# Performance work log

Measured on AMD Instinct MI355X. Metric: run time of the kernel, lower is better.

Reference implementation:

```python
import jax, jax.numpy as jnp
import numpy as np

N_HEAD = 16

def setup_inputs() -> dict:
    key = jax.random.key(0)
    k1, k2, k3 = jax.random.split(key, 3)
    B, T, C = 2, 2048, 2048
    x = jax.random.normal(k1, (B, T, C), dtype=jnp.float32)
    # torch Linear weights are [out, in]; init with small scale for stability
    w_attn = jax.random.normal(k2, (3 * C, C), dtype=jnp.float32) * 0.02
    b_attn = jnp.zeros((3 * C,), dtype=jnp.float32)
    w_proj = jax.random.normal(k3, (C, C), dtype=jnp.float32) * 0.02
    b_proj = jnp.zeros((C,), dtype=jnp.float32)
    return {"x": x, "w_attn": w_attn, "b_attn": b_attn, "w_proj": w_proj, "b_proj": b_proj}

def reference(x, w_attn, b_attn, w_proj, b_proj):
    B, T, C = x.shape
    nh = N_HEAD
    hs = C // nh
    # fused QKV projection (torch Linear: x @ W^T + b)
    qkv = x @ w_attn.T + b_attn                      # [B, T, 3C]
    q, k, v = jnp.split(qkv, 3, axis=2)
    # [B, nh, T, hs]
    q = q.reshape(B, T, nh, hs).transpose(0, 2, 1, 3)
    k = k.reshape(B, T, nh, hs).transpose(0, 2, 1, 3)
    v = v.reshape(B, T, nh, hs).transpose(0, 2, 1, 3)
    # causal scaled dot-product attention
    scale = 1.0 / jnp.sqrt(jnp.asarray(hs, dtype=x.dtype))
    logits = jnp.einsum("bhqd,bhkd->bhqk", q, k) * scale  # [B, nh, T, T]
    causal = jnp.tril(jnp.ones((T, T), dtype=bool))
    logits = jnp.where(causal, logits, jnp.finfo(logits.dtype).min)
    attn = jax.nn.softmax(logits, axis=-1)
    y = jnp.einsum("bhqk,bhkd->bhqd", attn, v)       # [B, nh, T, hs]
    y = y.transpose(0, 2, 1, 3).reshape(B, T, C)
    # output projection (resid_dropout is identity in eval / p=0)
    y = y @ w_proj.T + b_proj
    return y
```

## Files before the change

### kernel.cpp

```cpp
#include <hip/hip_runtime.h>
#include <stdint.h>

typedef __bf16 bf16_t;
typedef __bf16 bf16x8 __attribute__((ext_vector_type(8)));
typedef float f32x4 __attribute__((ext_vector_type(4)));
typedef unsigned short us16x8 __attribute__((ext_vector_type(8)));

#define MFMA16(a, b, c) __builtin_amdgcn_mfma_f32_16x16x32_bf16(a, b, c, 0, 0, 0)

__device__ __forceinline__ void stage16(const bf16_t* g, bf16_t* l) {
#if __has_builtin(__builtin_amdgcn_global_load_lds)
  __builtin_amdgcn_global_load_lds((__attribute__((address_space(1))) void*)g,
                                   (__attribute__((address_space(3))) void*)l, 16, 0, 0);
#else
  *(bf16x8*)l = *(const bf16x8*)g;
#endif
}

__global__ __launch_bounds__(256) void cvt_f32_to_bf16(const float* __restrict__ in,
                                                       bf16_t* __restrict__ out, int n8) {
  int i = blockIdx.x * 256 + threadIdx.x;
  if (i >= n8) return;
  const f32x4* p = (const f32x4*)(in + (size_t)i * 8);
  f32x4 a = p[0], b = p[1];
  bf16x8 o;
  o[0] = (bf16_t)a[0]; o[1] = (bf16_t)a[1]; o[2] = (bf16_t)a[2]; o[3] = (bf16_t)a[3];
  o[4] = (bf16_t)b[0]; o[5] = (bf16_t)b[1]; o[6] = (bf16_t)b[2]; o[7] = (bf16_t)b[3];
  *(bf16x8*)(out + (size_t)i * 8) = o;
}

template <int OUT_BF16>
__global__ __launch_bounds__(256) void gemm_nt(const bf16_t* __restrict__ A,
                                               const bf16_t* __restrict__ B,
                                               const float* __restrict__ bias,
                                               void* __restrict__ Cout,
                                               int M, int N, int K) {
  __shared__ bf16_t As[128 * 64];
  __shared__ bf16_t Bs[128 * 64];
  int tid = threadIdx.x;
  int l = tid & 63, w = tid >> 6;
  int wr = w >> 1, wc = w & 1;
  int nbn = N >> 7;
  int bm = blockIdx.x / nbn, bn = blockIdx.x % nbn;
  int l15 = l & 15, l4 = l >> 4, l7 = l & 7;

  f32x4 acc[4][4] = {};

  for (int ks = 0; ks < K; ks += 64) {
#pragma unroll
    for (int i = 0; i < 4; ++i) {
      int e = i * 256 + tid;
      int row = e >> 3, blk = e & 7;
      int col = ks + ((blk ^ (row & 7)) << 3);
      stage16(A + (size_t)(bm * 128 + row) * K + col, As + e * 8);
      stage16(B + (size_t)(bn * 128 + row) * K + col, Bs + e * 8);
    }
    __syncthreads();
#pragma unroll
    for (int kk = 0; kk < 2; ++kk) {
      bf16x8 af[4], bfr[4];
      int blk = (kk * 4 + l4) ^ l7;
#pragma unroll
      for (int m = 0; m < 4; ++m) {
        af[m] = *(const bf16x8*)(As + (wr * 64 + m * 16 + l15) * 64 + blk * 8);
        bfr[m] = *(const bf16x8*)(Bs + (wc * 64 + m * 16 + l15) * 64 + blk * 8);
      }
#pragma unroll
      for (int m = 0; m < 4; ++m)
#pragma unroll
        for (int n = 0; n < 4; ++n)
          acc[m][n] = MFMA16(af[m], bfr[n], acc[m][n]);
    }
    __syncthreads();
  }

  int rbase = bm * 128 + wr * 64 + (l4 << 2);
  int cbase = bn * 128 + wc * 64 + l15;
#pragma unroll
  for (int n = 0; n < 4; ++n) {
    float bv = bias[cbase + n * 16];
#pragma unroll
    for (int m = 0; m < 4; ++m)
#pragma unroll
      for (int r = 0; r < 4; ++r) {
        float v = acc[m][n][r] + bv;
        size_t off = (size_t)(rbase + m * 16 + r) * N + (cbase + n * 16);
        if (OUT_BF16) ((bf16_t*)Cout)[off] = (bf16_t)v;
        else ((float*)Cout)[off] = v;
      }
  }
}

__global__ __launch_bounds__(256, 2) void attn_fwd(const bf16_t* __restrict__ qkv,
                                                   bf16_t* __restrict__ att) {
  __shared__ bf16_t Kt[64 * 128];
  __shared__ bf16_t Vt[128 * 64];
  __shared__ bf16_t Pw[4][16 * 64];

  int bid = blockIdx.x;
  int pair = bid >> 5, bh = bid & 31;
  int h = bh & 15, b = bh >> 4;
  int tid = threadIdx.x;
  int l = tid & 63, w = tid >> 6;
  int l15 = l & 15, l4 = l >> 4, l7 = l & 7;
  const size_t LD = 6144;
  const bf16_t* base = qkv + (size_t)b * 2048 * LD;

#pragma unroll 1
  for (int phase = 0; phase < 2; ++phase) {
    int qt = phase ? 31 - pair : pair;
    int q0 = qt << 6;
    int wq0 = q0 + w * 16;

    bf16x8 qf[4];
#pragma unroll
    for (int kk = 0; kk < 4; ++kk)
      qf[kk] = *(const bf16x8*)(base + (size_t)(wq0 + l15) * LD + h * 128 + kk * 32 + l4 * 8);

    f32x4 acc[8] = {};
    float mrow[4], lrow[4];
#pragma unroll
    for (int r = 0; r < 4; ++r) { mrow[r] = -1e30f; lrow[r] = 0.f; }

    int nkt = qt + 1;
    for (int kt = 0; kt < nkt; ++kt) {
      int kb = kt << 6;
      const bf16_t* vg = base + (size_t)kb * LD + 4096 + h * 128;
      us16x8 va[2], vb[2];
#pragma unroll
      for (int p = 0; p < 2; ++p) {
        int g = p * 256 + tid;
        int kv = (g >> 4) << 1;
        int d0 = (g & 15) << 3;
        va[p] = *(const us16x8*)(vg + (size_t)kv * LD + d0);
        vb[p] = *(const us16x8*)(vg + (size_t)(kv + 1) * LD + d0);
      }
      const bf16_t* kg = base + (size_t)kb * LD + 2048 + h * 128;
#pragma unroll
      for (int i = 0; i < 4; ++i) {
        int e = i * 256 + tid;
        int row = e >> 4, blk = e & 15;
        int src = (blk ^ (row & 7)) << 3;
        stage16(kg + (size_t)row * LD + src, Kt + e * 8);
      }
#pragma unroll
      for (int p = 0; p < 2; ++p) {
        int g = p * 256 + tid;
        int kv = (g >> 4) << 1;
        int d0 = (g & 15) << 3;
        int k8 = kv >> 3, kr = kv & 7;
#pragma unroll
        for (int j = 0; j < 8; ++j) {
          int d = d0 + j;
          int swz = k8 ^ ((d ^ (d >> 3)) & 7);
          unsigned pack = (unsigned)va[p][j] | ((unsigned)vb[p][j] << 16);
          *(unsigned*)(&Vt[d * 64 + swz * 8 + kr]) = pack;
        }
      }
      __syncthreads();

      f32x4 s[4] = {};
      __builtin_amdgcn_s_setprio(1);
#pragma unroll
      for (int kk = 0; kk < 4; ++kk) {
        int blk = (kk * 4 + l4) ^ l7;
#pragma unroll
        for (int n = 0; n < 4; ++n) {
          bf16x8 kf = *(const bf16x8*)(Kt + (n * 16 + l15) * 128 + blk * 8);
          s[n] = MFMA16(qf[kk], kf, s[n]);
        }
      }
      __builtin_amdgcn_s_setprio(0);

      const float sc = 0.08838834764831845f;
      bool needMask = (kb + 63) > wq0;
      float scf[4];
#pragma unroll
      for (int r = 0; r < 4; ++r) {
        int q = wq0 + (l4 << 2) + r;
#pragma unroll
        for (int n = 0; n < 4; ++n) {
          float v = s[n][r] * sc;
          if (needMask && (kb + n * 16 + l15) > q) v = -1e30f;
          s[n][r] = v;
        }
        float mx = fmaxf(fmaxf(s[0][r], s[1][r]), fmaxf(s[2][r], s[3][r]));
        mx = fmaxf(mx, __shfl_xor(mx, 1));
        mx = fmaxf(mx, __shfl_xor(mx, 2));
        mx = fmaxf(mx, __shfl_xor(mx, 4));
        mx = fmaxf(mx, __shfl_xor(mx, 8));
        float mn = fmaxf(mrow[r], mx);
        float sf = __expf(mrow[r] - mn);
        mrow[r] = mn;
        scf[r] = sf;
        float rs = 0.f;
#pragma unroll
        for (int n = 0; n < 4; ++n) {
          float pv = __expf(s[n][r] - mn);
          s[n][r] = pv;
          rs += pv;
        }
        rs += __shfl_xor(rs, 1);
        rs += __shfl_xor(rs, 2);
        rs += __shfl_xor(rs, 4);
        rs += __shfl_xor(rs, 8);
        lrow[r] = lrow[r] * sf + rs;
      }
#pragma unroll
      for (int nd = 0; nd < 8; ++nd)
#pragma unroll
        for (int r = 0; r < 4; ++r)
          acc[nd][r] *= scf[r];
#pragma unroll
      for (int n = 0; n < 4; ++n) {
        int cb8 = n * 2 + (l15 >> 3);
#pragma unroll
        for (int r = 0; r < 4; ++r) {
          int row = (l4 << 2) + r;
          Pw[w][row * 64 + ((cb8 ^ (row & 7)) << 3) + l7] = (bf16_t)s[n][r];
        }
      }
      __builtin_amdgcn_s_setprio(1);
#pragma unroll
      for (int kk2 = 0; kk2 < 2; ++kk2) {
        bf16x8 pa = *(const bf16x8*)(&Pw[w][l15 * 64 + (((kk2 * 4 + l4) ^ l7) << 3)]);
#pragma unroll
        for (int nd = 0; nd < 8; ++nd) {
          int d = nd * 16 + l15;
          int swz = (kk2 * 4 + l4) ^ ((d ^ (d >> 3)) & 7);
          bf16x8 bv = *(const bf16x8*)(&Vt[d * 64 + swz * 8]);
          acc[nd] = MFMA16(pa, bv, acc[nd]);
        }
      }
      __builtin_amdgcn_s_setprio(0);
      __syncthreads();
    }

#pragma unroll
    for (int r = 0; r < 4; ++r) {
      float inv = 1.0f / lrow[r];
      size_t ro = (size_t)(b * 2048 + wq0 + (l4 << 2) + r) * 2048 + h * 128;
#pragma unroll
      for (int nd = 0; nd < 8; ++nd)
        att[ro + nd * 16 + l15] = (bf16_t)(acc[nd][r] * inv);
    }
  }
}

extern "C" void kernel_launch(void* const* d_in, const int* in_sizes, int n_in,
                              void* d_out, int out_size, void* d_ws, size_t ws_size,
                              hipStream_t stream) {
  (void)in_sizes; (void)n_in; (void)out_size; (void)ws_size;
  const float* x = (const float*)d_in[0];
  const float* w_attn = (const float*)d_in[1];
  const float* b_attn = (const float*)d_in[2];
  const float* w_proj = (const float*)d_in[3];
  const float* b_proj = (const float*)d_in[4];
  float* out = (float*)d_out;

  char* ws = (char*)d_ws;
  bf16_t* xb  = (bf16_t*)(ws);
  bf16_t* wab = (bf16_t*)(ws + 16777216);
  bf16_t* wpb = (bf16_t*)(ws + 41943040);
  bf16_t* qkv = (bf16_t*)(ws + 50331648);
  bf16_t* att = xb;

  cvt_f32_to_bf16<<<4096, 256, 0, stream>>>(x, xb, 1048576);
  cvt_f32_to_bf16<<<6144, 256, 0, stream>>>(w_attn, wab, 1572864);
  cvt_f32_to_bf16<<<2048, 256, 0, stream>>>(w_proj, wpb, 524288);

  gemm_nt<1><<<32 * 48, 256, 0, stream>>>(xb, wab, b_attn, qkv, 4096, 6144, 2048);

  attn_fwd<<<512, 256, 0, stream>>>(qkv, att);

  gemm_nt<0><<<32 * 16, 256, 0, stream>>>(att, wpb, b_proj, out, 4096, 2048, 2048);
}
```

Before: 287.0 us.

## Add 256x256 eight-wave ping-pong GEMM for QKV projection

Replaces the 128x128-tile QKV GEMM with a new 512-thread kernel using 256x256 tiles, double-buffered LDS staged through global_load_lds, and explicit barrier, waitcnt and priority scheduling. Each K step is split into quarter phases so async loads of the next tiles overlap MFMA work. Workgroup IDs are also remapped across eight groups for better cache locality. The aim is higher MFMA utilisation and fewer global loads per FLOP. In exchange it uses about 128 KB of LDS per block, relies on hand-tuned vmcnt values being correct, and the attention block change is only scoping.

```diff
diff --git a/kernel.cpp b/kernel.cpp
--- a/kernel.cpp
+++ b/kernel.cpp
@@ -7,14 +7,23 @@
 typedef unsigned short us16x8 __attribute__((ext_vector_type(8)));
 
 #define MFMA16(a, b, c) __builtin_amdgcn_mfma_f32_16x16x32_bf16(a, b, c, 0, 0, 0)
+#define BAR() __builtin_amdgcn_s_barrier()
+#define PRIO1() __builtin_amdgcn_s_setprio(1)
+#define PRIO0() __builtin_amdgcn_s_setprio(0)
+#define LGKM0()                                       \
+  do {                                                \
+    asm volatile("s_waitcnt lgkmcnt(0)" ::: "memory"); \
+    __builtin_amdgcn_sched_barrier(0);                \
+  } while (0)
+#define VMCNT(n)                                             \
+  do {                                                       \
+    asm volatile("s_waitcnt vmcnt(" #n ")" ::: "memory");    \
+    __builtin_amdgcn_sched_barrier(0);                       \
+  } while (0)
 
 __device__ __forceinline__ void stage16(const bf16_t* g, bf16_t* l) {
-#if __has_builtin(__builtin_amdgcn_global_load_lds)
   __builtin_amdgcn_global_load_lds((__attribute__((address_space(1))) void*)g,
                                    (__attribute__((address_space(3))) void*)l, 16, 0, 0);
-#else
-  *(bf16x8*)l = *(const bf16x8*)g;
-#endif
 }
 
 __global__ __launch_bounds__(256) void cvt_f32_to_bf16(const float* __restrict__ in,
@@ -27,6 +36,172 @@
   o[0] = (bf16_t)a[0]; o[1] = (bf16_t)a[1]; o[2] = (bf16_t)a[2]; o[3] = (bf16_t)a[3];
   o[4] = (bf16_t)b[0]; o[5] = (bf16_t)b[1]; o[6] = (bf16_t)b[2]; o[7] = (bf16_t)b[3];
   *(bf16x8*)(out + (size_t)i * 8) = o;
+}
+
+struct G8P {
+  const bf16_t* Ab;
+  const bf16_t* Bb;
+  bf16_t* SA;
+  bf16_t* SB;
+  int K, nk, tid, ardBase, brdBase, pb0, pb1;
+};
+
+__device__ __forceinline__ void stage_half(const bf16_t* src, bf16_t* dst, int K) {
+  stage16(src, dst);
+  stage16(src + ((size_t)K << 6), dst + 4096);
+}
+
+template <int CUR>
+__device__ __forceinline__ void g8p_group(const G8P& g, int t, bf16x8 (&aR)[4][2],
+                                          bf16x8 (&bR0)[2][2], bf16x8 (&bR1)[2][2],
+                                          f32x4 (&acc)[8][4]) {
+  const int t1 = (t + 1 < g.nk) ? t + 1 : g.nk - 1;
+  const int t2 = (t + 2 < g.nk) ? t + 2 : g.nk - 1;
+  bf16_t* SAc = g.SA + CUR * 16384;
+  bf16_t* SBc = g.SB + CUR * 16384;
+  bf16_t* SAn = g.SA + (1 - CUR) * 16384;
+
+#pragma unroll
+  for (int mi = 0; mi < 4; ++mi) {
+    aR[mi][0] = *(const bf16x8*)(SAc + g.ardBase + mi * 1024 + g.pb0);
+    aR[mi][1] = *(const bf16x8*)(SAc + g.ardBase + mi * 1024 + g.pb1);
+  }
+#pragma unroll
+  for (int ni = 0; ni < 2; ++ni) {
+    bR0[ni][0] = *(const bf16x8*)(SBc + g.brdBase + ni * 1024 + g.pb0);
+    bR0[ni][1] = *(const bf16x8*)(SBc + g.brdBase + ni * 1024 + g.pb1);
+  }
+  stage_half(g.Ab + (size_t)128 * g.K + (size_t)t1 * 64, SAn + 8192 + g.tid * 8, g.K);
+  BAR();
+  LGKM0();
+  PRIO1();
+#pragma unroll
+  for (int mi = 0; mi < 4; ++mi)
+#pragma unroll
+    for (int ni = 0; ni < 2; ++ni) {
+      acc[mi][ni] = MFMA16(aR[mi][0], bR0[ni][0], acc[mi][ni]);
+      acc[mi][ni] = MFMA16(aR[mi][1], bR0[ni][1], acc[mi][ni]);
+    }
+  PRIO0();
+  BAR();
+
+#pragma unroll
+  for (int ni = 0; ni < 2; ++ni) {
+    bR1[ni][0] = *(const bf16x8*)(SBc + g.brdBase + (2 + ni) * 1024 + g.pb0);
+    bR1[ni][1] = *(const bf16x8*)(SBc + g.brdBase + (2 + ni) * 1024 + g.pb1);
+  }
+  BAR();
+  LGKM0();
+  PRIO1();
+#pragma unroll
+  for (int mi = 0; mi < 4; ++mi)
+#pragma unroll
+    for (int ni = 0; ni < 2; ++ni) {
+      acc[mi][2 + ni] = MFMA16(aR[mi][0], bR1[ni][0], acc[mi][2 + ni]);
+      acc[mi][2 + ni] = MFMA16(aR[mi][1], bR1[ni][1], acc[mi][2 + ni]);
+    }
+  PRIO0();
+  BAR();
+
+#pragma unroll
+  for (int mi = 0; mi < 4; ++mi) {
+    aR[mi][0] = *(const bf16x8*)(SAc + g.ardBase + (4 + mi) * 1024 + g.pb0);
+    aR[mi][1] = *(const bf16x8*)(SAc + g.ardBase + (4 + mi) * 1024 + g.pb1);
+  }
+  stage_half(g.Bb + (size_t)t2 * 64, SBc + g.tid * 8, g.K);
+  BAR();
+  LGKM0();
+  PRIO1();
+#pragma unroll
+  for (int mi = 0; mi < 4; ++mi)
+#pragma unroll
+    for (int ni = 0; ni < 2; ++ni) {
+      acc[4 + mi][2 + ni] = MFMA16(aR[mi][0], bR1[ni][0], acc[4 + mi][2 + ni]);
+      acc[4 + mi][2 + ni] = MFMA16(aR[mi][1], bR1[ni][1], acc[4 + mi][2 + ni]);
+    }
+  PRIO0();
+  BAR();
+
+  stage_half(g.Ab + (size_t)t2 * 64, SAc + g.tid * 8, g.K);
+  stage_half(g.Bb + (size_t)128 * g.K + (size_t)t2 * 64, SBc + 8192 + g.tid * 8, g.K);
+  VMCNT(6);
+  BAR();
+  PRIO1();
+#pragma unroll
+  for (int mi = 0; mi < 4; ++mi)
+#pragma unroll
+    for (int ni = 0; ni < 2; ++ni) {
+      acc[4 + mi][ni] = MFMA16(aR[mi][0], bR0[ni][0], acc[4 + mi][ni]);
+      acc[4 + mi][ni] = MFMA16(aR[mi][1], bR0[ni][1], acc[4 + mi][ni]);
+    }
+  PRIO0();
+  BAR();
+}
+
+__global__ __launch_bounds__(512, 2) void gemm_nt_8p(const bf16_t* __restrict__ A,
+                                                     const bf16_t* __restrict__ B,
+                                                     const float* __restrict__ bias,
+                                                     bf16_t* __restrict__ C,
+                                                     int M, int N, int K) {
+  __shared__ bf16_t SA[2 * 256 * 64];
+  __shared__ bf16_t SB[2 * 256 * 64];
+  int tid = threadIdx.x;
+  int l = tid & 63, w = tid >> 6;
+  int l15 = l & 15, l4 = l >> 4, l7 = l & 7;
+  int wm = w >> 2, wn = w & 3;
+  int nbn = N >> 8;
+  int nwg = gridDim.x;
+  int bid = blockIdx.x;
+  int wg = (bid & 7) * (nwg >> 3) + (bid >> 3);
+  int bm = wg / nbn, bn = wg % nbn;
+
+  int row0 = tid >> 3;
+  int swc0 = ((tid & 7) ^ (row0 & 7)) << 3;
+  G8P g;
+  g.Ab = A + (size_t)(bm * 256 + row0) * K + swc0;
+  g.Bb = B + (size_t)(bn * 256 + row0) * K + swc0;
+  g.SA = SA; g.SB = SB;
+  g.K = K; g.nk = K >> 6; g.tid = tid;
+  g.ardBase = (wm * 128 + l15) * 64;
+  g.brdBase = (wn * 64 + l15) * 64;
+  g.pb0 = ((l4) ^ l7) << 3;
+  g.pb1 = ((4 + l4) ^ l7) << 3;
+
+  f32x4 acc[8][4] = {};
+  bf16x8 aR[4][2], bR0[2][2], bR1[2][2];
+
+  {
+    int t1 = (g.nk > 1) ? 1 : 0;
+    stage_half(g.Ab, SA + tid * 8, K);
+    stage_half(g.Bb, SB + tid * 8, K);
+    stage_half(g.Bb + (size_t)128 * K, SB + 8192 + tid * 8, K);
+    stage_half(g.Ab + (size_t)128 * K, SA + 8192 + tid * 8, K);
+    stage_half(g.Ab + (size_t)t1 * 64, SA + 16384 + tid * 8, K);
+    stage_half(g.Bb + (size_t)t1 * 64, SB + 16384 + tid * 8, K);
+    stage_half(g.Bb + (size_t)128 * K + (size_t)t1 * 64, SB + 16384 + 8192 + tid * 8, K);
+    VMCNT(6);
+    BAR();
+  }
+
+  for (int t = 0; t < g.nk; t += 2) {
+    g8p_group<0>(g, t, aR, bR0, bR1, acc);
+    g8p_group<1>(g, t + 1, aR, bR0, bR1, acc);
+  }
+  asm volatile("s_waitcnt vmcnt(0)" ::: "memory");
+
+  int rbase = bm * 256 + wm * 128 + (l4 << 2);
+  int cbase = bn * 256 + wn * 64 + l15;
+#pragma unroll
+  for (int ni = 0; ni < 4; ++ni) {
+    float bv = bias[cbase + ni * 16];
+#pragma unroll
+    for (int mi = 0; mi < 8; ++mi)
+#pragma unroll
+      for (int r = 0; r < 4; ++r) {
+        size_t off = (size_t)(rbase + mi * 16 + r) * N + (cbase + ni * 16);
+        C[off] = (bf16_t)(acc[mi][ni][r] + bv);
+      }
+  }
 }
 
 template <int OUT_BF16>
@@ -159,80 +334,82 @@
       }
       __syncthreads();
 
-      f32x4 s[4] = {};
-      __builtin_amdgcn_s_setprio(1);
-#pragma unroll
-      for (int kk = 0; kk < 4; ++kk) {
-        int blk = (kk * 4 + l4) ^ l7;
+      {
+        f32x4 s[4] = {};
+        __builtin_amdgcn_s_setprio(1);
+#pragma unroll
+        for (int kk = 0; kk < 4; ++kk) {
+          int blk = (kk * 4 + l4) ^ l7;
+#pragma unroll
+          for (int n = 0; n < 4; ++n) {
+            bf16x8 kf = *(const bf16x8*)(Kt + (n * 16 + l15) * 128 + blk * 8);
+            s[n] = MFMA16(qf[kk], kf, s[n]);
+          }
+        }
+        __builtin_amdgcn_s_setprio(0);
+
+        const float sc = 0.08838834764831845f;
+        bool needMask = (kb + 63) > wq0;
+        float scf[4];
+#pragma unroll
+        for (int r = 0; r < 4; ++r) {
+          int q = wq0 + (l4 << 2) + r;
+#pragma unroll
+          for (int n = 0; n < 4; ++n) {
+            float v = s[n][r] * sc;
+            if (needMask && (kb + n * 16 + l15) > q) v = -1e30f;
+            s[n][r] = v;
+          }
+          float mx = fmaxf(fmaxf(s[0][r], s[1][r]), fmaxf(s[2][r], s[3][r]));
+          mx = fmaxf(mx, __shfl_xor(mx, 1));
+          mx = fmaxf(mx, __shfl_xor(mx, 2));
+          mx = fmaxf(mx, __shfl_xor(mx, 4));
+          mx = fmaxf(mx, __shfl_xor(mx, 8));
+          float mn = fmaxf(mrow[r], mx);
+          float sf = __expf(mrow[r] - mn);
+          mrow[r] = mn;
+          scf[r] = sf;
+          float rs = 0.f;
+#pragma unroll
+          for (int n = 0; n < 4; ++n) {
+            float pv = __expf(s[n][r] - mn);
+            s[n][r] = pv;
+            rs += pv;
+          }
+          rs += __shfl_xor(rs, 1);
+          rs += __shfl_xor(rs, 2);
+          rs += __shfl_xor(rs, 4);
+          rs += __shfl_xor(rs, 8);
+          lrow[r] = lrow[r] * sf + rs;
+        }
+#pragma unroll
+        for (int nd = 0; nd < 8; ++nd)
+#pragma unroll
+          for (int r = 0; r < 4; ++r)
+            acc[nd][r] *= scf[r];
 #pragma unroll
         for (int n = 0; n < 4; ++n) {
-          bf16x8 kf = *(const bf16x8*)(Kt + (n * 16 + l15) * 128 + blk * 8);
-          s[n] = MFMA16(qf[kk], kf, s[n]);
+          int cb8 = n * 2 + (l15 >> 3);
+#pragma unroll
+          for (int r = 0; r < 4; ++r) {
+            int row = (l4 << 2) + r;
+            Pw[w][row * 64 + ((cb8 ^ (row & 7)) << 3) + l7] = (bf16_t)s[n][r];
+          }
         }
-      }
-      __builtin_amdgcn_s_setprio(0);
-
-      const float sc = 0.08838834764831845f;
-      bool needMask = (kb + 63) > wq0;
-      float scf[4];
-#pragma unroll
-      for (int r = 0; r < 4; ++r) {
-        int q = wq0 + (l4 << 2) + r;
-#pragma unroll
-        for (int n = 0; n < 4; ++n) {
-          float v = s[n][r] * sc;
-          if (needMask && (kb + n * 16 + l15) > q) v = -1e30f;
-          s[n][r] = v;
+        __builtin_amdgcn_s_setprio(1);
+#pragma unroll
+        for (int kk2 = 0; kk2 < 2; ++kk2) {
+          bf16x8 pa = *(const bf16x8*)(&Pw[w][l15 * 64 + (((kk2 * 4 + l4) ^ l7) << 3)]);
+#pragma unroll
+          for (int nd = 0; nd < 8; ++nd) {
+            int d = nd * 16 + l15;
+            int swz = (kk2 * 4 + l4) ^ ((d ^ (d >> 3)) & 7);
+            bf16x8 bv = *(const bf16x8*)(&Vt[d * 64 + swz * 8]);
+            acc[nd] = MFMA16(pa, bv, acc[nd]);
+          }
         }
-        float mx = fmaxf(fmaxf(s[0][r], s[1][r]), fmaxf(s[2][r], s[3][r]));
-        mx = fmaxf(mx, __shfl_xor(mx, 1));
-        mx = fmaxf(mx, __shfl_xor(mx, 2));
-        mx = fmaxf(mx, __shfl_xor(mx, 4));
-        mx = fmaxf(mx, __shfl_xor(mx, 8));
-        float mn = fmaxf(mrow[r], mx);
-        float sf = __expf(mrow[r] - mn);
-        mrow[r] = mn;
-        scf[r] = sf;
-        float rs = 0.f;
-#pragma unroll
-        for (int n = 0; n < 4; ++n) {
-          float pv = __expf(s[n][r] - mn);
-          s[n][r] = pv;
-          rs += pv;
-        }
-        rs += __shfl_xor(rs, 1);
-        rs += __shfl_xor(rs, 2);
-        rs += __shfl_xor(rs, 4);
-        rs += __shfl_xor(rs, 8);
-        lrow[r] = lrow[r] * sf + rs;
-      }
-#pragma unroll
-      for (int nd = 0; nd < 8; ++nd)
-#pragma unroll
-        for (int r = 0; r < 4; ++r)
-          acc[nd][r] *= scf[r];
-#pragma unroll
-      for (int n = 0; n < 4; ++n) {
-        int cb8 = n * 2 + (l15 >> 3);
-#pragma unroll
-        for (int r = 0; r < 4; ++r) {
-          int row = (l4 << 2) + r;
-          Pw[w][row * 64 + ((cb8 ^ (row & 7)) << 3) + l7] = (bf16_t)s[n][r];
-        }
-      }
-      __builtin_amdgcn_s_setprio(1);
-#pragma unroll
-      for (int kk2 = 0; kk2 < 2; ++kk2) {
-        bf16x8 pa = *(const bf16x8*)(&Pw[w][l15 * 64 + (((kk2 * 4 + l4) ^ l7) << 3)]);
-#pragma unroll
-        for (int nd = 0; nd < 8; ++nd) {
-          int d = nd * 16 + l15;
-          int swz = (kk2 * 4 + l4) ^ ((d ^ (d >> 3)) & 7);
-          bf16x8 bv = *(const bf16x8*)(&Vt[d * 64 + swz * 8]);
-          acc[nd] = MFMA16(pa, bv, acc[nd]);
-        }
-      }
-      __builtin_amdgcn_s_setprio(0);
+        __builtin_amdgcn_s_setprio(0);
+      }
       __syncthreads();
     }
 
@@ -269,7 +446,7 @@
   cvt_f32_to_bf16<<<6144, 256, 0, stream>>>(w_attn, wab, 1572864);
   cvt_f32_to_bf16<<<2048, 256, 0, stream>>>(w_proj, wpb, 524288);
 
-  gemm_nt<1><<<32 * 48, 256, 0, stream>>>(xb, wab, b_attn, qkv, 4096, 6144, 2048);
+  gemm_nt_8p<<<384, 512, 0, stream>>>(xb, wab, b_attn, qkv, 4096, 6144, 2048);
 
   attn_fwd<<<512, 256, 0, stream>>>(qkv, att);
 
```

After: 294.6 us. 1.03x slower.

## Replace GEMM with double-buffered 256x128 tile kernel using async LDS staging

Applied to the files above, without the earlier changes.

Rewrites both projection GEMMs as a 512-thread kernel with 256x128 output tiles and K split into 32-wide halves. Global-to-LDS loads for later K slices are issued ahead through a double-buffered ring, with explicit vmcnt/lgkmcnt waits and barriers so memory traffic overlaps the MFMA work. It also remaps block IDs in an XCD-aware order to improve L2 reuse. The attention kernel is only re-scoped into a block with no functional change. The hand-placed waitcnts rely on an exact count of outstanding loads, which makes the pipeline fragile if that count is off.

```diff
diff --git a/kernel.cpp b/kernel.cpp
--- a/kernel.cpp
+++ b/kernel.cpp
@@ -7,14 +7,23 @@
 typedef unsigned short us16x8 __attribute__((ext_vector_type(8)));
 
 #define MFMA16(a, b, c) __builtin_amdgcn_mfma_f32_16x16x32_bf16(a, b, c, 0, 0, 0)
+#define BAR() __builtin_amdgcn_s_barrier()
+#define PRIO1() __builtin_amdgcn_s_setprio(1)
+#define PRIO0() __builtin_amdgcn_s_setprio(0)
+#define LGKM0()                                        \
+  do {                                                 \
+    asm volatile("s_waitcnt lgkmcnt(0)" ::: "memory"); \
+    __builtin_amdgcn_sched_barrier(0);                 \
+  } while (0)
+#define VMCNT(n)                                          \
+  do {                                                    \
+    asm volatile("s_waitcnt vmcnt(" #n ")" ::: "memory"); \
+    __builtin_amdgcn_sched_barrier(0);                    \
+  } while (0)
 
 __device__ __forceinline__ void stage16(const bf16_t* g, bf16_t* l) {
-#if __has_builtin(__builtin_amdgcn_global_load_lds)
   __builtin_amdgcn_global_load_lds((__attribute__((address_space(1))) void*)g,
                                    (__attribute__((address_space(3))) void*)l, 16, 0, 0);
-#else
-  *(bf16x8*)l = *(const bf16x8*)g;
-#endif
 }
 
 __global__ __launch_bounds__(256) void cvt_f32_to_bf16(const float* __restrict__ in,
@@ -30,61 +39,103 @@
 }
 
 template <int OUT_BF16>
-__global__ __launch_bounds__(256) void gemm_nt(const bf16_t* __restrict__ A,
-                                               const bf16_t* __restrict__ B,
-                                               const float* __restrict__ bias,
-                                               void* __restrict__ Cout,
-                                               int M, int N, int K) {
-  __shared__ bf16_t As[128 * 64];
-  __shared__ bf16_t Bs[128 * 64];
-  int tid = threadIdx.x;
-  int l = tid & 63, w = tid >> 6;
-  int wr = w >> 1, wc = w & 1;
-  int nbn = N >> 7;
-  int bm = blockIdx.x / nbn, bn = blockIdx.x % nbn;
-  int l15 = l & 15, l4 = l >> 4, l7 = l & 7;
+__global__ __launch_bounds__(512, 2) void gemm_nt_p2(const bf16_t* __restrict__ A,
+                                                     const bf16_t* __restrict__ B,
+                                                     const float* __restrict__ bias,
+                                                     void* __restrict__ Cout,
+                                                     int M, int N, int K) {
+  __shared__ bf16_t SA[2 * 2 * 256 * 32];
+  __shared__ bf16_t SB[2 * 2 * 128 * 32];
+  const int tid = threadIdx.x;
+  const int l = tid & 63, w = tid >> 6;
+  const int l15 = l & 15, l4 = l >> 4;
+  const int wm = w >> 1, wn = w & 1;
+  const int nbm = M >> 8;
+  const int nwg = gridDim.x;
+  const int bid = blockIdx.x;
+  const int wg = (bid & 7) * (nwg >> 3) + (bid >> 3);
+  const int bn = wg / nbm, bm = wg % nbm;
+
+  const int sA0 = tid, sA1 = 512 + tid;
+  const int rA0 = sA0 >> 2, rA1 = sA1 >> 2, rB = tid >> 2;
+  const int cA0 = ((sA0 & 3) ^ ((rA0 >> 1) & 3)) << 3;
+  const int cA1 = ((sA1 & 3) ^ ((rA1 >> 1) & 3)) << 3;
+  const int cB = ((tid & 3) ^ ((rB >> 1) & 3)) << 3;
+  const bf16_t* gA0 = A + (size_t)(bm * 256 + rA0) * K + cA0;
+  const bf16_t* gA1 = A + (size_t)(bm * 256 + rA1) * K + cA1;
+  const bf16_t* gB = B + (size_t)(bn * 128 + rB) * K + cB;
+
+  int aoff[4], boff[4];
+#pragma unroll
+  for (int mi = 0; mi < 4; ++mi) {
+    int r = wm * 64 + mi * 16 + l15;
+    aoff[mi] = r * 32 + ((l4 ^ ((r >> 1) & 3)) << 3);
+  }
+#pragma unroll
+  for (int ni = 0; ni < 4; ++ni) {
+    int r = wn * 64 + ni * 16 + l15;
+    boff[ni] = r * 32 + ((l4 ^ ((r >> 1) & 3)) << 3);
+  }
 
   f32x4 acc[4][4] = {};
 
-  for (int ks = 0; ks < K; ks += 64) {
-#pragma unroll
-    for (int i = 0; i < 4; ++i) {
-      int e = i * 256 + tid;
-      int row = e >> 3, blk = e & 7;
-      int col = ks + ((blk ^ (row & 7)) << 3);
-      stage16(A + (size_t)(bm * 128 + row) * K + col, As + e * 8);
-      stage16(B + (size_t)(bn * 128 + row) * K + col, Bs + e * 8);
-    }
-    __syncthreads();
-#pragma unroll
-    for (int kk = 0; kk < 2; ++kk) {
-      bf16x8 af[4], bfr[4];
-      int blk = (kk * 4 + l4) ^ l7;
-#pragma unroll
-      for (int m = 0; m < 4; ++m) {
-        af[m] = *(const bf16x8*)(As + (wr * 64 + m * 16 + l15) * 64 + blk * 8);
-        bfr[m] = *(const bf16x8*)(Bs + (wc * 64 + m * 16 + l15) * 64 + blk * 8);
-      }
-#pragma unroll
-      for (int m = 0; m < 4; ++m)
-#pragma unroll
-        for (int n = 0; n < 4; ++n)
-          acc[m][n] = MFMA16(af[m], bfr[n], acc[m][n]);
-    }
-    __syncthreads();
-  }
-
-  int rbase = bm * 128 + wr * 64 + (l4 << 2);
-  int cbase = bn * 128 + wc * 64 + l15;
-#pragma unroll
-  for (int n = 0; n < 4; ++n) {
-    float bv = bias[cbase + n * 16];
-#pragma unroll
-    for (int m = 0; m < 4; ++m)
+  auto STAGE = [&](int tau, int h, int buf) {
+    const int koff = tau * 64 + h * 32;
+    stage16(gA0 + koff, SA + buf * 16384 + h * 8192 + sA0 * 8);
+    stage16(gA1 + koff, SA + buf * 16384 + h * 8192 + sA1 * 8);
+    stage16(gB + koff, SB + buf * 8192 + h * 4096 + tid * 8);
+  };
+
+  auto PHASE = [&](int buf, int h, int tauS, int hS, int bufS) {
+    bf16x8 aR[4], bR[4];
+#pragma unroll
+    for (int mi = 0; mi < 4; ++mi)
+      aR[mi] = *(const bf16x8*)(SA + buf * 16384 + h * 8192 + aoff[mi]);
+#pragma unroll
+    for (int ni = 0; ni < 4; ++ni)
+      bR[ni] = *(const bf16x8*)(SB + buf * 8192 + h * 4096 + boff[ni]);
+    STAGE(tauS, hS, bufS);
+    VMCNT(6);
+    BAR();
+    LGKM0();
+    PRIO1();
+#pragma unroll
+    for (int mi = 0; mi < 4; ++mi)
+#pragma unroll
+      for (int ni = 0; ni < 4; ++ni) acc[mi][ni] = MFMA16(aR[mi], bR[ni], acc[mi][ni]);
+    PRIO0();
+    BAR();
+  };
+
+  const int nk = K >> 6;
+  STAGE(0, 0, 0);
+  STAGE(0, 1, 0);
+  STAGE(1, 0, 1);
+  VMCNT(6);
+  BAR();
+
+  for (int t = 0; t < nk; t += 2) {
+    const int t1a = (t + 1 < nk) ? t + 1 : nk - 1;
+    const int t2a = (t + 2 < nk) ? t + 2 : nk - 1;
+    const int t3a = (t + 3 < nk) ? t + 3 : nk - 1;
+    PHASE(0, 0, t1a, 1, 1);
+    PHASE(0, 1, t2a, 0, 0);
+    PHASE(1, 0, t2a, 1, 0);
+    PHASE(1, 1, t3a, 0, 1);
+  }
+  VMCNT(0);
+
+  const int rbase = bm * 256 + wm * 64 + (l4 << 2);
+  const int cbase = bn * 128 + wn * 64 + l15;
+#pragma unroll
+  for (int ni = 0; ni < 4; ++ni) {
+    float bv = bias[cbase + ni * 16];
+#pragma unroll
+    for (int mi = 0; mi < 4; ++mi)
 #pragma unroll
       for (int r = 0; r < 4; ++r) {
-        float v = acc[m][n][r] + bv;
-        size_t off = (size_t)(rbase + m * 16 + r) * N + (cbase + n * 16);
+        float v = acc[mi][ni][r] + bv;
+        size_t off = (size_t)(rbase + mi * 16 + r) * N + (cbase + ni * 16);
         if (OUT_BF16) ((bf16_t*)Cout)[off] = (bf16_t)v;
         else ((float*)Cout)[off] = v;
       }
@@ -159,80 +210,82 @@
       }
       __syncthreads();
 
-      f32x4 s[4] = {};
-      __builtin_amdgcn_s_setprio(1);
-#pragma unroll
-      for (int kk = 0; kk < 4; ++kk) {
-        int blk = (kk * 4 + l4) ^ l7;
+      {
+        f32x4 s[4] = {};
+        __builtin_amdgcn_s_setprio(1);
+#pragma unroll
+        for (int kk = 0; kk < 4; ++kk) {
+          int blk = (kk * 4 + l4) ^ l7;
+#pragma unroll
+          for (int n = 0; n < 4; ++n) {
+            bf16x8 kf = *(const bf16x8*)(Kt + (n * 16 + l15) * 128 + blk * 8);
+            s[n] = MFMA16(qf[kk], kf, s[n]);
+          }
+        }
+        __builtin_amdgcn_s_setprio(0);
+
+        const float sc = 0.08838834764831845f;
+        bool needMask = (kb + 63) > wq0;
+        float scf[4];
+#pragma unroll
+        for (int r = 0; r < 4; ++r) {
+          int q = wq0 + (l4 << 2) + r;
+#pragma unroll
+          for (int n = 0; n < 4; ++n) {
+            float v = s[n][r] * sc;
+            if (needMask && (kb + n * 16 + l15) > q) v = -1e30f;
+            s[n][r] = v;
+          }
+          float mx = fmaxf(fmaxf(s[0][r], s[1][r]), fmaxf(s[2][r], s[3][r]));
+          mx = fmaxf(mx, __shfl_xor(mx, 1));
+          mx = fmaxf(mx, __shfl_xor(mx, 2));
+          mx = fmaxf(mx, __shfl_xor(mx, 4));
+          mx = fmaxf(mx, __shfl_xor(mx, 8));
+          float mn = fmaxf(mrow[r], mx);
+          float sf = __expf(mrow[r] - mn);
+          mrow[r] = mn;
+          scf[r] = sf;
+          float rs = 0.f;
+#pragma unroll
+          for (int n = 0; n < 4; ++n) {
+            float pv = __expf(s[n][r] - mn);
+            s[n][r] = pv;
+            rs += pv;
+          }
+          rs += __shfl_xor(rs, 1);
+          rs += __shfl_xor(rs, 2);
+          rs += __shfl_xor(rs, 4);
+          rs += __shfl_xor(rs, 8);
+          lrow[r] = lrow[r] * sf + rs;
+        }
+#pragma unroll
+        for (int nd = 0; nd < 8; ++nd)
+#pragma unroll
+          for (int r = 0; r < 4; ++r)
+            acc[nd][r] *= scf[r];
 #pragma unroll
         for (int n = 0; n < 4; ++n) {
-          bf16x8 kf = *(const bf16x8*)(Kt + (n * 16 + l15) * 128 + blk * 8);
-          s[n] = MFMA16(qf[kk], kf, s[n]);
-        }
-      }
-      __builtin_amdgcn_s_setprio(0);
-
-      const float sc = 0.08838834764831845f;
-      bool needMask = (kb + 63) > wq0;
-      float scf[4];
-#pragma unroll
-      for (int r = 0; r < 4; ++r) {
-        int q = wq0 + (l4 << 2) + r;
-#pragma unroll
-        for (int n = 0; n < 4; ++n) {
-          float v = s[n][r] * sc;
-          if (needMask && (kb + n * 16 + l15) > q) v = -1e30f;
-          s[n][r] = v;
-        }
-        float mx = fmaxf(fmaxf(s[0][r], s[1][r]), fmaxf(s[2][r], s[3][r]));
-        mx = fmaxf(mx, __shfl_xor(mx, 1));
-        mx = fmaxf(mx, __shfl_xor(mx, 2));
-        mx = fmaxf(mx, __shfl_xor(mx, 4));
-        mx = fmaxf(mx, __shfl_xor(mx, 8));
-        float mn = fmaxf(mrow[r], mx);
-        float sf = __expf(mrow[r] - mn);
-        mrow[r] = mn;
-        scf[r] = sf;
-        float rs = 0.f;
-#pragma unroll
-        for (int n = 0; n < 4; ++n) {
-          float pv = __expf(s[n][r] - mn);
-          s[n][r] = pv;
-          rs += pv;
-        }
-        rs += __shfl_xor(rs, 1);
-        rs += __shfl_xor(rs, 2);
-        rs += __shfl_xor(rs, 4);
-        rs += __shfl_xor(rs, 8);
-        lrow[r] = lrow[r] * sf + rs;
-      }
-#pragma unroll
-      for (int nd = 0; nd < 8; ++nd)
-#pragma unroll
-        for (int r = 0; r < 4; ++r)
-          acc[nd][r] *= scf[r];
-#pragma unroll
-      for (int n = 0; n < 4; ++n) {
-        int cb8 = n * 2 + (l15 >> 3);
-#pragma unroll
-        for (int r = 0; r < 4; ++r) {
-          int row = (l4 << 2) + r;
-          Pw[w][row * 64 + ((cb8 ^ (row & 7)) << 3) + l7] = (bf16_t)s[n][r];
-        }
-      }
-      __builtin_amdgcn_s_setprio(1);
-#pragma unroll
-      for (int kk2 = 0; kk2 < 2; ++kk2) {
-        bf16x8 pa = *(const bf16x8*)(&Pw[w][l15 * 64 + (((kk2 * 4 + l4) ^ l7) << 3)]);
-#pragma unroll
-        for (int nd = 0; nd < 8; ++nd) {
-          int d = nd * 16 + l15;
-          int swz = (kk2 * 4 + l4) ^ ((d ^ (d >> 3)) & 7);
-          bf16x8 bv = *(const bf16x8*)(&Vt[d * 64 + swz * 8]);
-          acc[nd] = MFMA16(pa, bv, acc[nd]);
-        }
-      }
-      __builtin_amdgcn_s_setprio(0);
+          int cb8 = n * 2 + (l15 >> 3);
+#pragma unroll
+          for (int r = 0; r < 4; ++r) {
+            int row = (l4 << 2) + r;
+            Pw[w][row * 64 + ((cb8 ^ (row & 7)) << 3) + l7] = (bf16_t)s[n][r];
+          }
+        }
+        __builtin_amdgcn_s_setprio(1);
+#pragma unroll
+        for (int kk2 = 0; kk2 < 2; ++kk2) {
+          bf16x8 pa = *(const bf16x8*)(&Pw[w][l15 * 64 + (((kk2 * 4 + l4) ^ l7) << 3)]);
+#pragma unroll
+          for (int nd = 0; nd < 8; ++nd) {
+            int d = nd * 16 + l15;
+            int swz = (kk2 * 4 + l4) ^ ((d ^ (d >> 3)) & 7);
+            bf16x8 bv = *(const bf16x8*)(&Vt[d * 64 + swz * 8]);
+            acc[nd] = MFMA16(pa, bv, acc[nd]);
+          }
+        }
+        __builtin_amdgcn_s_setprio(0);
+      }
       __syncthreads();
     }
 
@@ -269,9 +322,9 @@
   cvt_f32_to_bf16<<<6144, 256, 0, stream>>>(w_attn, wab, 1572864);
   cvt_f32_to_bf16<<<2048, 256, 0, stream>>>(w_proj, wpb, 524288);
 
-  gemm_nt<1><<<32 * 48, 256, 0, stream>>>(xb, wab, b_attn, qkv, 4096, 6144, 2048);
+  gemm_nt_p2<1><<<768, 512, 0, stream>>>(xb, wab, b_attn, qkv, 4096, 6144, 2048);
 
   attn_fwd<<<512, 256, 0, stream>>>(qkv, att);
 
-  gemm_nt<0><<<32 * 16, 256, 0, stream>>>(att, wpb, b_proj, out, 4096, 2048, 2048);
-}
+  gemm_nt_p2<0><<<256, 512, 0, stream>>>(att, wpb, b_proj, out, 4096, 2048, 2048);
+}
```

After: 310.0 us. 8.0% more time.
